# Kernel optimization log

Hardware: AMD Instinct MI355X
Metric: run time of the kernel (lower is better)

Reference implementation:

```python
import jax, jax.numpy as jnp
import numpy as np

NUM_PEAK = 28000
NUM_GENE = 12000
N_NODES = NUM_PEAK + NUM_GENE
N_EDGES = 640000
NUM_TOPICS = 100
T_HIDDEN = 512
EMB = 64
HID = 128  # 2 * emb_size, hidden_channels of GCN
BATCH = 256
BN_EPS = 1e-5


def setup_inputs() -> dict:
    key = jax.random.key(0)
    ks = iter(jax.random.split(key, 64))
    def nrm(shape, s=0.05):
        return jax.random.normal(next(ks), shape, dtype=jnp.float32) * s
    def unif(shape):
        return jax.random.uniform(next(ks), shape, dtype=jnp.float32)
    z = lambda *s: jnp.zeros(s, jnp.float32)
    o = lambda *s: jnp.ones(s, jnp.float32)
    inp = dict(
        Gene=unif((BATCH, NUM_GENE)),
        Gene_normalized=unif((BATCH, NUM_GENE)),
        Peak=unif((BATCH, NUM_PEAK)),
        Peak_normalized=unif((BATCH, NUM_PEAK)),
        feature_matrix=nrm((N_NODES, EMB), 1.0),
        # GATv2 layer 1 (EMB -> HID, heads=1)
        Wl1=nrm((HID, EMB)), bl1=z(HID), Wr1=nrm((HID, EMB)), br1=z(HID),
        att1=nrm((HID,), 0.1), bias1=z(HID),
        # GATv2 layer 2 (HID -> EMB)
        Wl2=nrm((EMB, HID)), bl2=z(EMB), Wr2=nrm((EMB, HID)), br2=z(EMB),
        att2=nrm((EMB,), 0.1), bias2=z(EMB),
        # gene encoder: Linear + ReLU + BN + Linear + ReLU + BN
        gW1=nrm((T_HIDDEN, NUM_GENE)), gb1=z(T_HIDDEN), gg1=o(T_HIDDEN), gbe1=z(T_HIDDEN),
        gW2=nrm((T_HIDDEN, T_HIDDEN)), gb2=z(T_HIDDEN), gg2=o(T_HIDDEN), gbe2=z(T_HIDDEN),
        # peak encoder
        pW1=nrm((T_HIDDEN, NUM_PEAK)), pb1=z(T_HIDDEN), pg1=o(T_HIDDEN), pbe1=z(T_HIDDEN),
        pW2=nrm((T_HIDDEN, T_HIDDEN)), pb2=z(T_HIDDEN), pg2=o(T_HIDDEN), pbe2=z(T_HIDDEN),
        mu_W=nrm((NUM_TOPICS, T_HIDDEN)), mu_b=z(NUM_TOPICS),
        ls_W=nrm((NUM_TOPICS, T_HIDDEN)), ls_b=z(NUM_TOPICS),
        alphas_W=nrm((NUM_TOPICS, EMB)),
        alphas_star_W=nrm((NUM_TOPICS, EMB)),
        edge_index=jax.random.randint(next(ks), (2, N_EDGES), 0, N_NODES),
    )
    return inp


def _batchnorm(h, gamma, beta):
    # training-style BN over batch axis (biased variance), eps=1e-5
    m = h.mean(axis=0)
    v = jnp.mean((h - m) ** 2, axis=0)
    return (h - m) * jax.lax.rsqrt(v + BN_EPS) * gamma + beta


def _gatv2(x, src, dst, Wl, bl, Wr, br, att, bias):
    # PyG GATv2Conv, heads=1: e_ij = att . leaky_relu(Wl x_j + Wr x_i),
    # softmax over incoming edges of i, out_i = sum_j alpha_ij * (Wl x_j) + bias
    xl = x @ Wl.T + bl            # [N, C]
    xr = x @ Wr.T + br            # [N, C]
    e = jax.nn.leaky_relu(xl[src] + xr[dst], negative_slope=0.2)  # [E, C]
    logit = e @ att               # [E]
    m = jax.ops.segment_max(logit, dst, num_segments=N_NODES)
    ex = jnp.exp(logit - m[dst])
    den = jax.ops.segment_sum(ex, dst, num_segments=N_NODES)
    alpha = ex / (den[dst] + 1e-16)
    out = jax.ops.segment_sum(alpha[:, None] * xl[src], dst, num_segments=N_NODES)
    return out + bias


def _encode(x, W1, b1, g1, be1, W2, b2, g2, be2, mu_W, mu_b, ls_W, ls_b):
    h = _batchnorm(jax.nn.relu(x @ W1.T + b1), g1, be1)
    h = _batchnorm(jax.nn.relu(h @ W2.T + b2), g2, be2)
    mu = h @ mu_W.T + mu_b
    logsigma = 2.0 * (h @ ls_W.T + ls_b)
    kl = -0.5 * jnp.sum(1.0 + logsigma - mu ** 2 - jnp.exp(logsigma), axis=-1).mean()
    return mu, kl


def reference(Gene, Gene_normalized, Peak, Peak_normalized, feature_matrix,
              Wl1, bl1, Wr1, br1, att1, bias1,
              Wl2, bl2, Wr2, br2, att2, bias2,
              gW1, gb1, gg1, gbe1, gW2, gb2, gg2, gbe2,
              pW1, pb1, pg1, pbe1, pW2, pb2, pg2, pbe2,
              mu_W, mu_b, ls_W, ls_b, alphas_W, alphas_star_W, edge_index):
    # ---- variational encoders (eval mode: dropout off, theta from mu) ----
    mu_d, kl_d = _encode(Gene_normalized, gW1, gb1, gg1, gbe1, gW2, gb2, gg2, gbe2,
                         mu_W, mu_b, ls_W, ls_b)
    mu_j, kl_j = _encode(Peak_normalized, pW1, pb1, pg1, pbe1, pW2, pb2, pg2, pbe2,
                         mu_W, mu_b, ls_W, ls_b)
    theta_d = jax.nn.softmax(mu_d, axis=-1)   # [B, K]
    theta_j = jax.nn.softmax(mu_j, axis=-1)
    kld_theta = kl_d + kl_j

    # ---- GCN embedding: two GATv2Conv layers with self-loops ----
    loops = jnp.arange(N_NODES)
    src = jnp.concatenate([edge_index[0], loops])
    dst = jnp.concatenate([edge_index[1], loops])
    h = jax.nn.relu(_gatv2(feature_matrix, src, dst, Wl1, bl1, Wr1, br1, att1, bias1))
    emb = _gatv2(h, src, dst, Wl2, bl2, Wr2, br2, att2, bias2)
    emb = jax.nn.relu(emb)  # theta_act applied in forward
    eta_matrix = emb[:NUM_PEAK]   # [num_peak, EMB]
    rho_matrix = emb[NUM_PEAK:]   # [num_gene, EMB]

    # ---- topic-word matrices: softmax over genes/peaks (dim=0), transposed ----
    beta_gene = jax.nn.softmax(rho_matrix @ alphas_W.T, axis=0).T        # [K, num_gene]
    beta_peak = jax.nn.softmax(eta_matrix @ alphas_star_W.T, axis=0).T   # [K, num_peak]

    # ---- decode + reconstruction loss ----
    preds_gene = jnp.log(theta_d @ beta_gene + 1e-6)
    preds_peak = jnp.log(theta_j @ beta_peak + 1e-6)
    recon = (-(preds_gene * Gene).sum(-1) - (preds_peak * Peak).sum(-1)).mean()
    return recon, kld_theta
```

## Files before the change

### kernel.cpp

```cpp
#include <hip/hip_runtime.h>
#include <cstdint>
#include <cstddef>

using u16 = unsigned short;
using u32 = unsigned int;
typedef __attribute__((ext_vector_type(8))) short bf16x8;
typedef __attribute__((ext_vector_type(4))) float f32x4;

static constexpr int NUM_PEAK = 28000;
static constexpr int NUM_GENE = 12000;
static constexpr int N_NODES  = NUM_PEAK + NUM_GENE;
static constexpr int N_EDGES  = 640000;
static constexpr int E_TOTAL  = N_EDGES + N_NODES;
static constexpr int NT       = 100;
static constexpr int NT2      = 200;
static constexpr int NTP      = 128;
static constexpr int TH       = 512;
static constexpr int EMB      = 64;
static constexpr int HID      = 128;
static constexpr int BATCH    = 256;
static constexpr int SCAN_CHUNK = 1024;
static constexpr int SCAN_NB  = (N_NODES + SCAN_CHUNK - 1) / SCAN_CHUNK;
static constexpr int ENC_CH   = 1280;
static constexpr int KPG      = 12032;
static constexpr int KPP      = 28032;
static constexpr int KSPG     = (NUM_GENE + ENC_CH - 1) / ENC_CH;
static constexpr int KSPP     = (NUM_PEAK + ENC_CH - 1) / ENC_CH;
static constexpr int ENC1B    = 8 * 4 * (KSPG + KSPP);
static constexpr int DEGB     = (E_TOTAL + 255) / 256;
static constexpr int PADGB    = BATCH * KPG / 8 / 256;
static constexpr int PADPB    = BATCH * KPP / 8 / 256;
static constexpr int CS_ROWS  = 128;
static constexpr int NBMAX    = (NUM_PEAK + CS_ROWS - 1) / CS_ROWS;
#define BN_EPS 1e-5f

__device__ __forceinline__ u16 f2bf(float f) {
  u32 b = __float_as_uint(f);
  return (u16)((b + 0x7FFFu + ((b >> 16) & 1u)) >> 16);
}

struct CvtJobs {
  const float* src[12];
  u16* dst[12];
  u32 n[12];
  u32 start[12];
  int count;
};

__device__ void dev_cvt_all(const CvtJobs& J, int bid) {
  int seg = 0;
  while (seg + 1 < J.count && bid >= (int)J.start[seg + 1]) ++seg;
  const float* __restrict__ src = J.src[seg];
  u16* __restrict__ dst = J.dst[seg];
  const u32 n = J.n[seg];
  const u32 i = (u32)(bid - J.start[seg]) * 2048u + threadIdx.x * 8u;
  if (i + 8 <= n) {
    float4 a = *(const float4*)(src + i);
    float4 b = *(const float4*)(src + i + 4);
    ushort4 o0{f2bf(a.x), f2bf(a.y), f2bf(a.z), f2bf(a.w)};
    ushort4 o1{f2bf(b.x), f2bf(b.y), f2bf(b.z), f2bf(b.w)};
    *(ushort4*)(dst + i) = o0;
    *(ushort4*)(dst + i + 4) = o1;
  } else {
    for (u32 j = i; j < n; ++j) dst[j] = f2bf(src[j]);
  }
}

__device__ void dev_cvt_pad(const float* __restrict__ src, u16* __restrict__ dst,
                            int K, int Kp, int bid) {
  const size_t i = ((size_t)bid * 256 + threadIdx.x) * 8;
  const int col = (int)(i % Kp);
  const size_t row = i / Kp;
  ushort4 o0{0, 0, 0, 0}, o1{0, 0, 0, 0};
  if (col + 8 <= K) {
    const float* s = src + row * K + col;
    float4 a = *(const float4*)s;
    float4 b = *(const float4*)(s + 4);
    o0 = ushort4{f2bf(a.x), f2bf(a.y), f2bf(a.z), f2bf(a.w)};
    o1 = ushort4{f2bf(b.x), f2bf(b.y), f2bf(b.z), f2bf(b.w)};
  }
  *(ushort4*)(dst + i) = o0;
  *(ushort4*)(dst + i + 4) = o1;
}

__device__ void dev_deg_count(const int* __restrict__ ei, int* __restrict__ deg,
                              int* __restrict__ pos, int bid) {
  const int e = bid * 256 + threadIdx.x;
  if (e >= E_TOTAL) return;
  const int d = (e < N_EDGES) ? ei[N_EDGES + e] : e - N_EDGES;
  pos[e] = atomicAdd(&deg[d], 1);
}

__device__ void dev_csr_scatter(const int* __restrict__ ei,
                                const int* __restrict__ row_ptr,
                                const int* __restrict__ pos,
                                int* __restrict__ csr_src, int bid) {
  const int e = bid * 256 + threadIdx.x;
  if (e >= E_TOTAL) return;
  int s, d;
  if (e < N_EDGES) { s = ei[e]; d = ei[N_EDGES + e]; }
  else { s = d = e - N_EDGES; }
  csr_src[row_ptr[d] + pos[e]] = s;
}

__global__ __launch_bounds__(256) void megaA(
    const int* ei, int* deg, int* pos,
    const float* GeneN, u16* GeneNb, const float* PeakN, u16* PeakNb,
    CvtJobs J) {
  const int bid = blockIdx.x;
  if (bid < DEGB) dev_deg_count(ei, deg, pos, bid);
  else if (bid < DEGB + PADGB) dev_cvt_pad(GeneN, GeneNb, NUM_GENE, KPG, bid - DEGB);
  else if (bid < DEGB + PADGB + PADPB) dev_cvt_pad(PeakN, PeakNb, NUM_PEAK, KPP, bid - DEGB - PADGB);
  else dev_cvt_all(J, bid - DEGB - PADGB - PADPB);
}

struct GP {
  const u16* A; const u16* B; float* C; u16* Cb; const float* bias;
  int M, N, K;
};

__device__ void dev_gemm_bt(const GP g, int bxx, int byy, char* smem) {
  u16 (*As)[40] = (u16(*)[40])smem;
  u16 (*Bs)[40] = (u16(*)[40])(smem + 64 * 40 * 2);
  const int M = g.M, N = g.N, K = g.K;
  const int tid = threadIdx.x;
  const int bm = byy * 64, bn = bxx * 64;
  if (bm >= M || bn >= N) return;
  const int w = tid >> 6, lane = tid & 63;
  const int wm = (w >> 1) * 32, wn = (w & 1) * 32;
  const int fr = lane & 15;
  const int ks = (lane >> 4) * 8;
  const int srow = tid >> 2, sseg = (tid & 3) * 8;
  f32x4 acc[2][2] = {};
  for (int kt = 0; kt < K; kt += 32) {
    const int gk = kt + sseg;
    {
      const int gm = bm + srow;
      bf16x8 v = {0, 0, 0, 0, 0, 0, 0, 0};
      if (gm < M) v = *(const bf16x8*)(g.A + (size_t)gm * K + gk);
      *(bf16x8*)&As[srow][sseg] = v;
    }
    {
      const int gn = bn + srow;
      bf16x8 v = {0, 0, 0, 0, 0, 0, 0, 0};
      if (gn < N) v = *(const bf16x8*)(g.B + (size_t)gn * K + gk);
      *(bf16x8*)&Bs[srow][sseg] = v;
    }
    __syncthreads();
    bf16x8 a0 = *(const bf16x8*)&As[wm + fr][ks];
    bf16x8 a1 = *(const bf16x8*)&As[wm + 16 + fr][ks];
    bf16x8 b0 = *(const bf16x8*)&Bs[wn + fr][ks];
    bf16x8 b1 = *(const bf16x8*)&Bs[wn + 16 + fr][ks];
    acc[0][0] = __builtin_amdgcn_mfma_f32_16x16x32_bf16(a0, b0, acc[0][0], 0, 0, 0);
    acc[0][1] = __builtin_amdgcn_mfma_f32_16x16x32_bf16(a0, b1, acc[0][1], 0, 0, 0);
    acc[1][0] = __builtin_amdgcn_mfma_f32_16x16x32_bf16(a1, b0, acc[1][0], 0, 0, 0);
    acc[1][1] = __builtin_amdgcn_mfma_f32_16x16x32_bf16(a1, b1, acc[1][1], 0, 0, 0);
    __syncthreads();
  }
#pragma unroll
  for (int fi = 0; fi < 2; ++fi)
#pragma unroll
    for (int fj = 0; fj < 2; ++fj)
#pragma unroll
      for (int r = 0; r < 4; ++r) {
        const int row = bm + wm + fi * 16 + (lane >> 4) * 4 + r;
        const int col = bn + wn + fj * 16 + fr;
        if (row < M && col < N) {
          const float v = acc[fi][fj][r];
          if (g.Cb) g.Cb[(size_t)row * N + col] = f2bf(v + (g.bias ? g.bias[col] : 0.f));
          else g.C[(size_t)row * N + col] = v + (g.bias ? g.bias[col] : 0.f);
        }
      }
}

__device__ __forceinline__ int swz64(int row, int colu16) {
  return row * 64 + ((((colu16 >> 3) ^ row) & 7) << 3) + (colu16 & 7);
}

__device__ void dev_enc1(
    const u16* __restrict__ A0, const float* __restrict__ B0, float* __restrict__ P0,
    const u16* __restrict__ A1, const float* __restrict__ B1, float* __restrict__ P1,
    int bid, char* smem) {
  const int cpx = ENC1B >> 3;
  const int f2 = (bid & 7) * cpx + (bid >> 3);
  const int bx = f2 % 8;
  const int by = (f2 / 8) % 4;
  const int bz = f2 / 32;
  const bool second = (bz >= KSPG);
  const u16* __restrict__ A = second ? A1 : A0;
  const float* __restrict__ B = second ? B1 : B0;
  float* __restrict__ P = second ? P1 : P0;
  const int K = second ? NUM_PEAK : NUM_GENE;
  const int Kp = second ? KPP : KPG;
  const int zz = second ? bz - KSPG : bz;
  const int k0 = zz * ENC_CH;
  const int k1 = min(K, k0 + ENC_CH);
  u16* As = (u16*)smem;
  u16* Bs = (u16*)(smem + 8192);
  const int tid = threadIdx.x;
  const int bm = by * 64;
  const int bn = bx * 64;
  const int w = tid >> 6, lane = tid & 63;
  const int wm = w * 16;
  const int fr = lane & 15, g = lane >> 4;
  const int ar = tid >> 2, acol = (tid & 3) * 16;
  const int br = tid >> 2, bcol = (tid & 3) * 16;
  const u16* Abase = A + (size_t)(bm + ar) * Kp + acol;
  const float* Bbase = B + (size_t)(bn + br) * K + bcol;

  bf16x8 rA0, rA1;
  float4 rB0, rB1, rB2, rB3;
  auto LD = [&](int kt) {
    const u16* sa = Abase + kt;
    rA0 = *(const bf16x8*)(sa);
    rA1 = *(const bf16x8*)(sa + 8);
    if (kt + bcol + 16 <= K) {
      const float* sb = Bbase + kt;
      rB0 = *(const float4*)(sb);
      rB1 = *(const float4*)(sb + 4);
      rB2 = *(const float4*)(sb + 8);
      rB3 = *(const float4*)(sb + 12);
    } else {
      rB0 = float4{0.f, 0.f, 0.f, 0.f}; rB1 = rB0; rB2 = rB0; rB3 = rB0;
    }
  };
  auto ST = [&]() {
    *(bf16x8*)&As[swz64(ar, acol)] = rA0;
    *(bf16x8*)&As[swz64(ar, acol + 8)] = rA1;
    ushort4 p0{f2bf(rB0.x), f2bf(rB0.y), f2bf(rB0.z), f2bf(rB0.w)};
    ushort4 p1{f2bf(rB1.x), f2bf(rB1.y), f2bf(rB1.z), f2bf(rB1.w)};
    ushort4 p2{f2bf(rB2.x), f2bf(rB2.y), f2bf(rB2.z), f2bf(rB2.w)};
    ushort4 p3{f2bf(rB3.x), f2bf(rB3.y), f2bf(rB3.z), f2bf(rB3.w)};
    const int b0 = swz64(br, bcol);
    const int b1 = swz64(br, bcol + 8);
    *(ushort4*)&Bs[b0] = p0;
    *(ushort4*)&Bs[b0 + 4] = p1;
    *(ushort4*)&Bs[b1] = p2;
    *(ushort4*)&Bs[b1 + 4] = p3;
  };

  f32x4 acc[4] = {};
  LD(k0);
  ST();
  for (int kt = k0; kt < k1; kt += 64) {
    __syncthreads();
    const bool more = (kt + 64 < k1);
    if (more) LD(kt + 64);
#pragma unroll
    for (int s = 0; s < 2; ++s) {
      const int kc = s * 32 + g * 8;
      bf16x8 a = *(const bf16x8*)&As[swz64(wm + fr, kc)];
#pragma unroll
      for (int fj = 0; fj < 4; ++fj) {
        bf16x8 b = *(const bf16x8*)&Bs[swz64(fj * 16 + fr, kc)];
        acc[fj] = __builtin_amdgcn_mfma_f32_16x16x32_bf16(a, b, acc[fj], 0, 0, 0);
      }
    }
    __syncthreads();
    if (more) ST();
  }
  float* Pz = P + (size_t)zz * TH * 256;
  const int row = bm + wm + g * 4;
#pragma unroll
  for (int fj = 0; fj < 4; ++fj) {
    const int col = bn + fj * 16 + fr;
    *(f32x4*)&Pz[(size_t)col * 256 + row] = acc[fj];
  }
}

template <int C>
__device__ void dev_gat(
    const u16* __restrict__ xl, const u16* __restrict__ xr,
    const float* __restrict__ att, const float* __restrict__ bias,
    const int* __restrict__ row_ptr, const int* __restrict__ csr_src,
    u16* __restrict__ out_b, int blk) {
  constexpr int CPL = C / 8;
  constexpr int W = CPL / 2;
  const int lane = threadIdx.x & 63;
  const int g = lane >> 3, li = lane & 7;
  const int d = blk * 4 + ((int)threadIdx.x >> 6);
  if (d >= N_NODES) return;
  const int c0 = li * CPL;
  float xrv[CPL], attv[CPL], acc[CPL];
  {
    const u32* xrw = (const u32*)(xr + (size_t)d * C + c0);
#pragma unroll
    for (int i = 0; i < W; ++i) {
      const u32 wv = xrw[i];
      xrv[2 * i]     = __uint_as_float(wv << 16);
      xrv[2 * i + 1] = __uint_as_float(wv & 0xffff0000u);
    }
  }
#pragma unroll
  for (int i = 0; i < CPL; ++i) { attv[i] = att[c0 + i]; acc[i] = 0.f; }
  float m = -INFINITY, den = 0.f;
  const int end = row_ptr[d + 1];
  int p = row_ptr[d] + g;
  int s = (p < end) ? csr_src[p] : 0;
  u32 w[W];
  {
    const u32* sw = (const u32*)(xl + (size_t)s * C + c0);
#pragma unroll
    for (int i = 0; i < W; ++i) w[i] = sw[i];
  }
  while (p < end) {
    const int sn = (p + 8 < end) ? csr_src[p + 8] : 0;
    u32 wn[W];
    {
      const u32* sw = (const u32*)(xl + (size_t)sn * C + c0);
#pragma unroll
      for (int i = 0; i < W; ++i) wn[i] = sw[i];
    }
    float xlv[CPL];
#pragma unroll
    for (int i = 0; i < W; ++i) {
      xlv[2 * i]     = __uint_as_float(w[i] << 16);
      xlv[2 * i + 1] = __uint_as_float(w[i] & 0xffff0000u);
    }
    float part = 0.f;
#pragma unroll
    for (int i = 0; i < CPL; ++i) {
      float x = xlv[i] + xrv[i];
      x = (x > 0.f) ? x : 0.2f * x;
      part += x * attv[i];
    }
    part += __shfl_xor(part, 1);
    part += __shfl_xor(part, 2);
    part += __shfl_xor(part, 4);
    const float nm = fmaxf(m, part);
    const float scale = __expf(m - nm);
    const float ex = __expf(part - nm);
    den = den * scale + ex;
#pragma unroll
    for (int i = 0; i < CPL; ++i) acc[i] = acc[i] * scale + ex * xlv[i];
    m = nm;
    p += 8;
#pragma unroll
    for (int i = 0; i < W; ++i) w[i] = wn[i];
  }
  float M = m;
  M = fmaxf(M, __shfl_xor(M, 8));
  M = fmaxf(M, __shfl_xor(M, 16));
  M = fmaxf(M, __shfl_xor(M, 32));
  const float gs = __expf(m - M);
  den *= gs;
  den += __shfl_xor(den, 8);
  den += __shfl_xor(den, 16);
  den += __shfl_xor(den, 32);
  const float inv = 1.f / (den + 1e-16f);
  float va[CPL];
#pragma unroll
  for (int i = 0; i < CPL; ++i) {
    float a = acc[i] * gs;
    a += __shfl_xor(a, 8);
    a += __shfl_xor(a, 16);
    a += __shfl_xor(a, 32);
    va[i] = a;
  }
  if (g == 0) {
    u32* dst = (u32*)(out_b + (size_t)d * C + c0);
#pragma unroll
    for (int i = 0; i < W; ++i) {
      const u16 lo = f2bf(fmaxf(va[2 * i] * inv + bias[c0 + 2 * i], 0.f));
      const u16 hi = f2bf(fmaxf(va[2 * i + 1] * inv + bias[c0 + 2 * i + 1], 0.f));
      dst[i] = (u32)lo | ((u32)hi << 16);
    }
  }
}

__device__ void dev_bn_body(float v, const float* gma, const float* be, int c,
                            u16* ob, float* red) {
  const int r = threadIdx.x;
  red[r] = v; __syncthreads();
  for (int s = BATCH / 2; s > 0; s >>= 1) { if (r < s) red[r] += red[r + s]; __syncthreads(); }
  const float mean = red[0] * (1.f / BATCH);
  __syncthreads();
  const float d = v - mean;
  red[r] = d * d; __syncthreads();
  for (int s = BATCH / 2; s > 0; s >>= 1) { if (r < s) red[r] += red[r + s]; __syncthreads(); }
  const float var = red[0] * (1.f / BATCH);
  ob[(size_t)r * TH + c] = f2bf(d * rsqrtf(var + BN_EPS) * gma[c] + be[c]);
}

__device__ void dev_bn_part(
    int cg, const float* __restrict__ PG, int nzG, const float* bg,
    const float* gg, const float* beg, u16* og,
    const float* __restrict__ PP, int nzP, const float* bp,
    const float* gp, const float* bep, u16* op, float* red) {
  int c = cg;
  const float *P, *b, *gma, *be; u16* ob; int nz;
  if (c < TH) { P = PG; nz = nzG; b = bg; gma = gg; be = beg; ob = og; }
  else { c -= TH; P = PP; nz = nzP; b = bp; gma = gp; be = bep; ob = op; }
  const int r = threadIdx.x;
  float v = 0.f;
  const float* base = P + (size_t)c * 256 + r;
  for (int z = 0; z < nz; ++z) v += base[(size_t)z * TH * 256];
  v = fmaxf(v + b[c], 0.f);
  dev_bn_body(v, gma, be, c, ob, red);
}

__device__ void dev_bn2(
    int cg, const float* __restrict__ Hg, const float* bg,
    const float* gg, const float* beg, u16* og,
    const float* __restrict__ Hp, const float* bp,
    const float* gp, const float* bep, u16* op, float* red) {
  int c = cg;
  const float *H, *b, *gma, *be; u16* ob;
  if (c < TH) { H = Hg; b = bg; gma = gg; be = beg; ob = og; }
  else { c -= TH; H = Hp; b = bp; gma = gp; be = bep; ob = op; }
  const int r = threadIdx.x;
  float v = fmaxf(H[(size_t)r * TH + c] + b[c], 0.f);
  dev_bn_body(v, gma, be, c, ob, red);
}

__device__ void dev_row_kl(
    int b, int which, const float* __restrict__ mld, const float* __restrict__ mlj,
    const float* mu_b, const float* ls_b,
    u16* thd, u16* thj, float* kl_out, float* red) {
  const float* ml = which ? mlj : mld;
  u16* thb = which ? thj : thd;
  const int t = threadIdx.x;
  const bool act = (t < NT);
  float mu = 0.f, ls = 0.f, term = 0.f;
  if (act) {
    mu = ml[(size_t)b * NT2 + t] + mu_b[t];
    ls = 2.f * (ml[(size_t)b * NT2 + NT + t] + ls_b[t]);
    term = 1.f + ls - mu * mu - expf(ls);
  }
  red[t] = act ? term : 0.f; __syncthreads();
  for (int s = 64; s > 0; s >>= 1) { if (t < s) red[t] += red[t + s]; __syncthreads(); }
  if (t == 0) atomicAdd(kl_out, -0.5f * red[0] * (1.f / BATCH));
  __syncthreads();
  red[t] = act ? mu : -INFINITY; __syncthreads();
  for (int s = 64; s > 0; s >>= 1) { if (t < s) red[t] = fmaxf(red[t], red[t + s]); __syncthreads(); }
  const float mx = red[0];
  __syncthreads();
  const float e = act ? expf(mu - mx) : 0.f;
  red[t] = e; __syncthreads();
  for (int s = 64; s > 0; s >>= 1) { if (t < s) red[t] += red[t + s]; __syncthreads(); }
  thb[(size_t)b * NTP + t] = act ? f2bf(e / red[0]) : (u16)0;
}

__device__ void dev_col_stats(
    int bx, int sec, const float* __restrict__ Lg, const float* __restrict__ Lp,
    float* __restrict__ bstats) {
  const float* L = sec ? Lp : Lg;
  const int M = sec ? NUM_PEAK : NUM_GENE;
  const int r0 = bx * CS_ROWS;
  const int c = threadIdx.x;
  if (c >= NT || r0 >= M) return;
  const int rend = min(r0 + CS_ROWS, M);
  float m = -INFINITY, s = 0.f;
  for (int r = r0; r < rend; ++r) {
    const float v = L[(size_t)r * NT + c];
    const float nm = fmaxf(m, v);
    s = s * __expf(m - nm) + __expf(v - nm);
    m = nm;
  }
  float* bs = bstats + (((size_t)sec * NT + c) * NBMAX + bx) * 2;
  bs[0] = m;
  bs[1] = s;
}

__global__ __launch_bounds__(256) void mega1(
    const u16* A0, const float* B0, float* P0,
    const u16* A1, const float* B1, float* P1,
    GP l, GP r,
    const int* ei, const int* row_ptr, const int* pos, int* csr_src) {
  __shared__ __align__(16) char smem[20480];
  const int bid = blockIdx.x;
  if (bid < ENC1B) {
    dev_enc1(A0, B0, P0, A1, B1, P1, bid, smem);
  } else if (bid < ENC1B + 2500) {
    const int sub = bid - ENC1B;
    const GP& g = (sub >= 1250) ? r : l;
    const int rem = sub % 1250;
    dev_gemm_bt(g, rem % 2, rem / 2, smem);
  } else {
    dev_csr_scatter(ei, row_ptr, pos, csr_src, bid - ENC1B - 2500);
  }
}

__global__ __launch_bounds__(256) void mega2(
    const float* PG, int nzG, const float* bg, const float* gg, const float* beg, u16* og,
    const float* PP, int nzP, const float* bp, const float* gp, const float* bep, u16* op,
    const u16* xl, const u16* xr, const float* att, const float* bias,
    const int* row_ptr, const int* csr_src, u16* out_b) {
  __shared__ float red[256];
  const int bid = blockIdx.x;
  if (bid < 2 * TH)
    dev_bn_part(bid, PG, nzG, bg, gg, beg, og, PP, nzP, bp, gp, bep, op, red);
  else
    dev_gat<HID>(xl, xr, att, bias, row_ptr, csr_src, out_b, bid - 2 * TH);
}

__global__ __launch_bounds__(256) void mega3(GP eg, GP ep, GP l, GP r) {
  __shared__ __align__(16) char smem[20480];
  const int bid = blockIdx.x;
  if (bid < 64) {
    const int z = bid >> 5, rem = bid & 31;
    dev_gemm_bt(z ? ep : eg, rem & 7, rem >> 3, smem);
  } else {
    const int sub = bid - 64;
    const GP& g = (sub >= 625) ? r : l;
    dev_gemm_bt(g, 0, sub % 625, smem);
  }
}

__global__ __launch_bounds__(256) void mega4(
    const float* Hg, const float* bg, const float* gg, const float* beg, u16* og,
    const float* Hp, const float* bp, const float* gp, const float* bep, u16* op,
    const u16* xl, const u16* xr, const float* att, const float* bias,
    const int* row_ptr, const int* csr_src, u16* out_b) {
  __shared__ float red[256];
  const int bid = blockIdx.x;
  if (bid < 2 * TH)
    dev_bn2(bid, Hg, bg, gg, beg, og, Hp, bp, gp, bep, op, red);
  else
    dev_gat<EMB>(xl, xr, att, bias, row_ptr, csr_src, out_b, bid - 2 * TH);
}

__global__ __launch_bounds__(256) void mega5(GP hg, GP hp, GP tg, GP tp) {
  __shared__ __align__(16) char smem[20480];
  const int bid = blockIdx.x;
  if (bid < 32) {
    const int z = bid >> 4, rem = bid & 15;
    dev_gemm_bt(z ? hp : hg, rem & 3, rem >> 2, smem);
  } else {
    const int sub = bid - 32;
    const GP& g = (sub >= 876) ? tp : tg;
    const int rem = sub % 876;
    dev_gemm_bt(g, rem & 1, rem >> 1, smem);
  }
}

__global__ __launch_bounds__(128) void mega6(
    const float* mld, const float* mlj, const float* mu_b, const float* ls_b,
    u16* thd, u16* thj, float* kl_out,
    const float* Lg, const float* Lp, float* bstats) {
  __shared__ float red[128];
  const int bid = blockIdx.x;
  if (bid < 2 * BATCH)
    dev_row_kl(bid % BATCH, bid / BATCH, mld, mlj, mu_b, ls_b, thd, thj, kl_out, red);
  else {
    const int sub = bid - 2 * BATCH;
    dev_col_stats(sub % NBMAX, sub / NBMAX, Lg, Lp, bstats);
  }
}

__global__ __launch_bounds__(256) void scan_part(
    const int* __restrict__ deg, int* __restrict__ bsum) {
  const int base = blockIdx.x * SCAN_CHUNK + threadIdx.x * 4;
  int s = 0;
#pragma unroll
  for (int i = 0; i < 4; ++i) {
    const int idx = base + i;
    if (idx < N_NODES) s += deg[idx];
  }
  for (int o = 32; o > 0; o >>= 1) s += __shfl_down(s, o);
  __shared__ int ws[4];
  if ((threadIdx.x & 63) == 0) ws[threadIdx.x >> 6] = s;
  __syncthreads();
  if (threadIdx.x == 0) bsum[blockIdx.x] = ws[0] + ws[1] + ws[2] + ws[3];
}

__global__ __launch_bounds__(64) void scan_bsum(int* __restrict__ bsum) {
  if (threadIdx.x == 0) {
    int run = 0;
    for (int i = 0; i < SCAN_NB; ++i) { int v = bsum[i]; bsum[i] = run; run += v; }
  }
}

__global__ __launch_bounds__(256) void scan_final(
    const int* __restrict__ deg, const int* __restrict__ bsum,
    int* __restrict__ row_ptr) {
  const int t = threadIdx.x;
  const int base = blockIdx.x * SCAN_CHUNK + t * 4;
  int v[4], s = 0;
#pragma unroll
  for (int i = 0; i < 4; ++i) {
    const int idx = base + i;
    v[i] = (idx < N_NODES) ? deg[idx] : 0;
    s += v[i];
  }
  const int lane = t & 63, w = t >> 6;
  int x = s;
  for (int o = 1; o < 64; o <<= 1) {
    int y = __shfl_up(x, o);
    if (lane >= o) x += y;
  }
  __shared__ int wtot[4];
  if (lane == 63) wtot[w] = x;
  __syncthreads();
  int woff = 0;
  for (int i = 0; i < w; ++i) woff += wtot[i];
  int excl = bsum[blockIdx.x] + woff + x - s;
#pragma unroll
  for (int i = 0; i < 4; ++i) {
    const int idx = base + i;
    if (idx < N_NODES) { row_ptr[idx] = excl; excl += v[i]; }
  }
  if (blockIdx.x == 0 && t == 0) row_ptr[N_NODES] = E_TOTAL;
}

__global__ __launch_bounds__(64) void col_merge(
    const float* __restrict__ bstats, int nbG, int nbP,
    float* __restrict__ mstat, float* __restrict__ istat) {
  const bool sec = (blockIdx.y != 0);
  const int nb = sec ? nbP : nbG;
  const int c = blockIdx.x;
  const int l = threadIdx.x;
  const float* bs = bstats + ((size_t)blockIdx.y * NT + c) * NBMAX * 2;
  float m = -INFINITY, s = 0.f;
  for (int b = l; b < nb; b += 64) {
    const float mb = bs[b * 2];
    const float sb = bs[b * 2 + 1];
    const float nm = fmaxf(m, mb);
    s = s * __expf(m - nm) + sb * __expf(mb - nm);
    m = nm;
  }
#pragma unroll
  for (int o = 32; o > 0; o >>= 1) {
    const float mo = __shfl_xor(m, o);
    const float so = __shfl_xor(s, o);
    const float nm = fmaxf(m, mo);
    s = s * __expf(m - nm) + so * __expf(mo - nm);
    m = nm;
  }
  if (l == 0) {
    mstat[blockIdx.y * NT + c] = m;
    istat[blockIdx.y * NT + c] = 1.f / s;
  }
}

__global__ __launch_bounds__(256) void beta_norm(
    const float* __restrict__ Lg, const float* __restrict__ Lp,
    const float* __restrict__ mstat, const float* __restrict__ istat,
    u16* __restrict__ og, u16* __restrict__ op) {
  const float* L = blockIdx.y ? Lp : Lg;
  const int M = blockIdx.y ? NUM_PEAK : NUM_GENE;
  const float* mxg = mstat + blockIdx.y * NT;
  const float* ivg = istat + blockIdx.y * NT;
  u16* o = blockIdx.y ? op : og;
  __shared__ float mx[NT], inv[NT];
  for (int i = threadIdx.x; i < NT; i += 256) { mx[i] = mxg[i]; inv[i] = ivg[i]; }
  __syncthreads();
  const size_t total = (size_t)M * NTP;
  size_t i = (size_t)blockIdx.x * 256 + threadIdx.x;
  const size_t stride = (size_t)gridDim.x * 256;
  for (; i < total; i += stride) {
    const int c = (int)(i & (NTP - 1));
    u16 v = 0;
    if (c < NT) {
      const size_t r = i >> 7;
      v = f2bf(__expf(L[r * NT + c] - mx[c]) * inv[c]);
    }
    o[i] = v;
  }
}

__global__ __launch_bounds__(256) void recon_fused(
    const u16* __restrict__ thg, const u16* __restrict__ betag,
    const float* __restrict__ Xg, int Ng, int tiles_g,
    const u16* __restrict__ thp, const u16* __restrict__ betap,
    const float* __restrict__ Xp, int Np, float* __restrict__ partials) {
  __shared__ float pred[64][65];
  __shared__ float wsum[4];
  int ct = blockIdx.x;
  const u16* A; const u16* B; const float* X; int N;
  if (ct < tiles_g) { A = thg; B = betag; X = Xg; N = Ng; }
  else { ct -= tiles_g; A = thp; B = betap; X = Xp; N = Np; }
  const int bm = blockIdx.y * 64, bn = ct * 64;
  const int tid = threadIdx.x, w = tid >> 6, lane = tid & 63;
  const int wm = (w >> 1) * 32, wn = (w & 1) * 32;
  const int fr = lane & 15, ks = (lane >> 4) * 8;
  const u16* Ar0 = A + (size_t)(bm + wm + fr) * NTP;
  const u16* Ar1 = A + (size_t)(bm + wm + 16 + fr) * NTP;
  bf16x8 a0[4], a1[4];
#pragma unroll
  for (int kt = 0; kt < 4; ++kt) {
    a0[kt] = *(const bf16x8*)(Ar0 + kt * 32 + ks);
    a1[kt] = *(const bf16x8*)(Ar1 + kt * 32 + ks);
  }
  const int gn0 = min(bn + wn + fr, N - 1);
  const int gn1 = min(bn + wn + 16 + fr, N - 1);
  const u16* Br0 = B + (size_t)gn0 * NTP;
  const u16* Br1 = B + (size_t)gn1 * NTP;
  f32x4 acc[2][2] = {};
#pragma unroll
  for (int kt = 0; kt < 4; ++kt) {
    bf16x8 b0 = *(const bf16x8*)(Br0 + kt * 32 + ks);
    bf16x8 b1 = *(const bf16x8*)(Br1 + kt * 32 + ks);
    acc[0][0] = __builtin_amdgcn_mfma_f32_16x16x32_bf16(a0[kt], b0, acc[0][0], 0, 0, 0);
    acc[0][1] = __builtin_amdgcn_mfma_f32_16x16x32_bf16(a0[kt], b1, acc[0][1], 0, 0, 0);
    acc[1][0] = __builtin_amdgcn_mfma_f32_16x16x32_bf16(a1[kt], b0, acc[1][0], 0, 0, 0);
    acc[1][1] = __builtin_amdgcn_mfma_f32_16x16x32_bf16(a1[kt], b1, acc[1][1], 0, 0, 0);
  }
#pragma unroll
  for (int fi = 0; fi < 2; ++fi)
#pragma unroll
    for (int fj = 0; fj < 2; ++fj)
#pragma unroll
      for (int r = 0; r < 4; ++r)
        pred[wm + fi * 16 + (lane >> 4) * 4 + r][wn + fj * 16 + fr] = acc[fi][fj][r];
  __syncthreads();
  float local = 0.f;
  if (bn + 64 <= N) {
#pragma unroll
    for (int k = 0; k < 4; ++k) {
      const int j = k * 1024 + tid * 4;
      const int row = j >> 6, col = j & 63;
      const float4 xv = *(const float4*)(X + (size_t)(bm + row) * N + bn + col);
      local += xv.x * __logf(pred[row][col + 0] + 1e-6f);
      local += xv.y * __logf(pred[row][col + 1] + 1e-6f);
      local += xv.z * __logf(pred[row][col + 2] + 1e-6f);
      local += xv.w * __logf(pred[row][col + 3] + 1e-6f);
    }
  } else {
#pragma unroll
    for (int k = 0; k < 16; ++k) {
      const int idx = k * 256 + tid, row = idx >> 6, col = idx & 63;
      if (bn + col < N)
        local += X[(size_t)(bm + row) * N + bn + col] * __logf(pred[row][col] + 1e-6f);
    }
  }
  for (int o = 32; o > 0; o >>= 1) local += __shfl_down(local, o);
  if (lane == 0) wsum[w] = local;
  __syncthreads();
  if (tid == 0)
    partials[(size_t)blockIdx.y * gridDim.x + blockIdx.x] =
        wsum[0] + wsum[1] + wsum[2] + wsum[3];
}

__global__ __launch_bounds__(256) void final_recon(
    const float* __restrict__ partials, int n, float* __restrict__ out) {
  float s = 0.f;
  for (int i = threadIdx.x; i < n; i += 256) s += partials[i];
  __shared__ float red[256];
  red[threadIdx.x] = s; __syncthreads();
  for (int o = 128; o > 0; o >>= 1) {
    if (threadIdx.x < o) red[threadIdx.x] += red[threadIdx.x + o];
    __syncthreads();
  }
  if (threadIdx.x == 0) out[0] = -red[0] * (1.f / BATCH);
}

extern "C" void kernel_launch(void* const* d_in, const int* in_sizes, int n_in,
                              void* d_out, int out_size, void* d_ws, size_t ws_size,
                              hipStream_t stream) {
  const float* Gene  = (const float*)d_in[0];
  const float* GeneN = (const float*)d_in[1];
  const float* Peak  = (const float*)d_in[2];
  const float* PeakN = (const float*)d_in[3];
  const float* feat  = (const float*)d_in[4];
  const float* Wl1 = (const float*)d_in[5];  const float* bl1 = (const float*)d_in[6];
  const float* Wr1 = (const float*)d_in[7];  const float* br1 = (const float*)d_in[8];
  const float* att1 = (const float*)d_in[9]; const float* bias1 = (const float*)d_in[10];
  const float* Wl2 = (const float*)d_in[11]; const float* bl2 = (const float*)d_in[12];
  const float* Wr2 = (const float*)d_in[13]; const float* br2 = (const float*)d_in[14];
  const float* att2 = (const float*)d_in[15]; const float* bias2 = (const float*)d_in[16];
  const float* gW1 = (const float*)d_in[17]; const float* gb1 = (const float*)d_in[18];
  const float* gg1 = (const float*)d_in[19]; const float* gbe1 = (const float*)d_in[20];
  const float* gW2 = (const float*)d_in[21]; const float* gb2 = (const float*)d_in[22];
  const float* gg2 = (const float*)d_in[23]; const float* gbe2 = (const float*)d_in[24];
  const float* pW1 = (const float*)d_in[25]; const float* pb1 = (const float*)d_in[26];
  const float* pg1 = (const float*)d_in[27]; const float* pbe1 = (const float*)d_in[28];
  const float* pW2 = (const float*)d_in[29]; const float* pb2 = (const float*)d_in[30];
  const float* pg2 = (const float*)d_in[31]; const float* pbe2 = (const float*)d_in[32];
  const float* mu_W = (const float*)d_in[33]; const float* mu_b = (const float*)d_in[34];
  const float* ls_W = (const float*)d_in[35]; const float* ls_b = (const float*)d_in[36];
  const float* alphas_W = (const float*)d_in[37];
  const float* alphas_star_W = (const float*)d_in[38];
  const int* ei = (const int*)d_in[39];
  float* out = (float*)d_out;
  (void)in_sizes; (void)n_in; (void)ws_size;

  char* base = (char*)d_ws;
  size_t off = 0;
  auto A = [&](size_t bytes) { void* p = base + off; off += (bytes + 255) & ~(size_t)255; return p; };
  int* deg     = (int*)A((size_t)N_NODES * 4);
  int* row_ptr = (int*)A((size_t)(N_NODES + 1) * 4);
  int* bsum    = (int*)A((size_t)(SCAN_NB + 1) * 4);
  int* pos     = (int*)A((size_t)E_TOTAL * 4);
  int* csr_src = (int*)A((size_t)E_TOTAL * 4);
  float* CpartG = (float*)A((size_t)KSPG * TH * 256 * 4);
  float* CpartP = (float*)A((size_t)KSPP * TH * 256 * 4);
  float* h2g = (float*)A((size_t)BATCH * TH * 4);
  float* h2p = (float*)A((size_t)BATCH * TH * 4);
  u16* h1gb = (u16*)A((size_t)BATCH * TH * 2);
  u16* h2gb = (u16*)A((size_t)BATCH * TH * 2);
  u16* h1pb = (u16*)A((size_t)BATCH * TH * 2);
  u16* h2pb = (u16*)A((size_t)BATCH * TH * 2);
  float* ml_d = (float*)A((size_t)BATCH * NT2 * 4);
  float* ml_j = (float*)A((size_t)BATCH * NT2 * 4);
  u16* th_db = (u16*)A((size_t)BATCH * NTP * 2);
  u16* th_jb = (u16*)A((size_t)BATCH * NTP * 2);
  float* lgg = (float*)A((size_t)NUM_GENE * NT * 4);
  float* lgp = (float*)A((size_t)NUM_PEAK * NT * 4);
  u16* betagb = (u16*)A((size_t)NUM_GENE * NTP * 2);
  u16* betapb = (u16*)A((size_t)NUM_PEAK * NTP * 2);
  u16* featb = (u16*)A((size_t)N_NODES * EMB * 2);
  u16* gW2b = (u16*)A((size_t)TH * TH * 2);
  u16* pW2b = (u16*)A((size_t)TH * TH * 2);
  u16* mlWb = (u16*)A((size_t)NT2 * TH * 2);
  u16* Wl1b = (u16*)A((size_t)HID * EMB * 2);
  u16* Wr1b = (u16*)A((size_t)HID * EMB * 2);
  u16* Wl2b = (u16*)A((size_t)EMB * HID * 2);
  u16* Wr2b = (u16*)A((size_t)EMB * HID * 2);
  u16* aWb  = (u16*)A((size_t)NT * EMB * 2);
  u16* aSWb = (u16*)A((size_t)NT * EMB * 2);
  u16* agg1b = (u16*)A((size_t)N_NODES * HID * 2);
  u16* embb  = (u16*)A((size_t)N_NODES * EMB * 2);
  float* mstat = (float*)A(2 * NT * 4);
  float* istat = (float*)A(2 * NT * 4);
  float* bstats = (float*)A((size_t)2 * NT * NBMAX * 2 * 4);
  float* partials = (float*)A(4096 * 4);
  u16* xl1b = (u16*)A((size_t)N_NODES * HID * 2);
  u16* xr1b = (u16*)A((size_t)N_NODES * HID * 2);
  u16* xl2b = (u16*)A((size_t)N_NODES * EMB * 2);
  u16* xr2b = (u16*)A((size_t)N_NODES * EMB * 2);
  u16* GeneNb = (u16*)A((size_t)BATCH * KPG * 2);
  u16* PeakNb = (u16*)A((size_t)BATCH * KPP * 2);

  auto cdiv = [](int a, int b) { return (a + b - 1) / b; };
  auto Z = [&](void* p, size_t bytes) { hipMemsetAsync(p, 0, bytes, stream); };

  Z(d_out, (size_t)out_size * sizeof(float));
  Z(deg, (size_t)N_NODES * 4);

  int cvtallB;
  {
    CvtJobs J = {};
    int c = 0; u32 blocks = 0;
    auto add = [&](const float* s, u16* d, size_t n) {
      J.src[c] = s; J.dst[c] = d; J.n[c] = (u32)n; J.start[c] = blocks;
      blocks += (u32)((n + 2047) / 2048); ++c;
    };
    add(gW2, gW2b, (size_t)TH * TH);
    add(pW2, pW2b, (size_t)TH * TH);
    add(mu_W, mlWb, (size_t)NT * TH);
    add(ls_W, mlWb + (size_t)NT * TH, (size_t)NT * TH);
    add(feat, featb, (size_t)N_NODES * EMB);
    add(Wl1, Wl1b, (size_t)HID * EMB);
    add(Wr1, Wr1b, (size_t)HID * EMB);
    add(Wl2, Wl2b, (size_t)EMB * HID);
    add(Wr2, Wr2b, (size_t)EMB * HID);
    add(alphas_W, aWb, (size_t)NT * EMB);
    add(alphas_star_W, aSWb, (size_t)NT * EMB);
    J.count = c;
    cvtallB = (int)blocks;
    megaA<<<DEGB + PADGB + PADPB + cvtallB, 256, 0, stream>>>(
        ei, deg, pos, GeneN, GeneNb, PeakN, PeakNb, J);
  }

  scan_part<<<SCAN_NB, 256, 0, stream>>>(deg, bsum);
  scan_bsum<<<1, 64, 0, stream>>>(bsum);
  scan_final<<<SCAN_NB, 256, 0, stream>>>(deg, bsum, row_ptr);

  {
    GP l = {featb, Wl1b, nullptr, xl1b, bl1, N_NODES, HID, EMB};
    GP r = {featb, Wr1b, nullptr, xr1b, br1, N_NODES, HID, EMB};
    mega1<<<ENC1B + 2500 + DEGB, 256, 0, stream>>>(
        GeneNb, gW1, CpartG, PeakNb, pW1, CpartP, l, r,
        ei, row_ptr, pos, csr_src);
  }

  mega2<<<2 * TH + N_NODES / 4, 256, 0, stream>>>(
      CpartG, KSPG, gb1, gg1, gbe1, h1gb,
      CpartP, KSPP, pb1, pg1, pbe1, h1pb,
      xl1b, xr1b, att1, bias1, row_ptr, csr_src, agg1b);

  {
    GP eg = {h1gb, gW2b, h2g, nullptr, nullptr, BATCH, TH, TH};
    GP ep = {h1pb, pW2b, h2p, nullptr, nullptr, BATCH, TH, TH};
    GP l  = {agg1b, Wl2b, nullptr, xl2b, bl2, N_NODES, EMB, HID};
    GP r  = {agg1b, Wr2b, nullptr, xr2b, br2, N_NODES, EMB, HID};
    mega3<<<64 + 1250, 256, 0, stream>>>(eg, ep, l, r);
  }

  mega4<<<2 * TH + N_NODES / 4, 256, 0, stream>>>(
      h2g, gb2, gg2, gbe2, h2gb,
      h2p, pb2, pg2, pbe2, h2pb,
      xl2b, xr2b, att2, bias2, row_ptr, csr_src, embb);

  {
    GP hg = {h2gb, mlWb, ml_d, nullptr, nullptr, BATCH, NT2, TH};
    GP hp = {h2pb, mlWb, ml_j, nullptr, nullptr, BATCH, NT2, TH};
    GP tg = {embb + (size_t)NUM_PEAK * EMB, aWb, lgg, nullptr, nullptr, NUM_GENE, NT, EMB};
    GP tp = {embb, aSWb, lgp, nullptr, nullptr, NUM_PEAK, NT, EMB};
    mega5<<<32 + 2 * 2 * 438, 256, 0, stream>>>(hg, hp, tg, tp);
  }

  mega6<<<2 * BATCH + 2 * NBMAX, 128, 0, stream>>>(
      ml_d, ml_j, mu_b, ls_b, th_db, th_jb, out + 1, lgg, lgp, bstats);

  const int nbG = cdiv(NUM_GENE, CS_ROWS);
  const int nbP = cdiv(NUM_PEAK, CS_ROWS);
  col_merge<<<dim3(NT, 2), 64, 0, stream>>>(bstats, nbG, nbP, mstat, istat);
  beta_norm<<<dim3(1024, 2), 256, 0, stream>>>(lgg, lgp, mstat, istat, betagb, betapb);

  const int tiles_g = cdiv(NUM_GENE, 64);
  const int tiles_p = cdiv(NUM_PEAK, 64);
  const int tiles = tiles_g + tiles_p;
  recon_fused<<<dim3(tiles, 4), 256, 0, stream>>>(
      th_db, betagb, Gene, NUM_GENE, tiles_g,
      th_jb, betapb, Peak, NUM_PEAK, partials);
  final_recon<<<1, 256, 0, stream>>>(partials, tiles * 4, out);
}
```

Baseline: 332.1 us.

## Fuse beta softmax normalization into recon GEMM and pad logits to 128 columns

Removes the separate beta_norm kernel, which read the fp32 logits and wrote a padded bf16 beta matrix. The recon kernel now reads the fp32 logits directly and applies exp(x - max) * inv_sum before converting to bf16 for the MFMA operands. To allow aligned float4 loads, the logit GEMM output gets a 128-column stride through a new ldc field, and col_stats is updated to match. This saves a launch and a full write and read of beta. In exchange, the exp work is repeated across the 4 batch-row blocks, and recon loads twice the bytes per element (fp32 instead of bf16).

```diff
diff --git a/kernel.cpp b/kernel.cpp
--- a/kernel.cpp
+++ b/kernel.cpp
@@ -116,7 +116,7 @@
 
 struct GP {
   const u16* A; const u16* B; float* C; u16* Cb; const float* bias;
-  int M, N, K;
+  int M, N, K, ldc;
 };
 
 __device__ void dev_gemm_bt(const GP g, int bxx, int byy, char* smem) {
@@ -167,8 +167,8 @@
         const int col = bn + wn + fj * 16 + fr;
         if (row < M && col < N) {
           const float v = acc[fi][fj][r];
-          if (g.Cb) g.Cb[(size_t)row * N + col] = f2bf(v + (g.bias ? g.bias[col] : 0.f));
-          else g.C[(size_t)row * N + col] = v + (g.bias ? g.bias[col] : 0.f);
+          if (g.Cb) g.Cb[(size_t)row * g.ldc + col] = f2bf(v + (g.bias ? g.bias[col] : 0.f));
+          else g.C[(size_t)row * g.ldc + col] = v + (g.bias ? g.bias[col] : 0.f);
         }
       }
 }
@@ -452,7 +452,7 @@
   const int rend = min(r0 + CS_ROWS, M);
   float m = -INFINITY, s = 0.f;
   for (int r = r0; r < rend; ++r) {
-    const float v = L[(size_t)r * NT + c];
+    const float v = L[(size_t)r * NTP + c];
     const float nm = fmaxf(m, v);
     s = s * __expf(m - nm) + __expf(v - nm);
     m = nm;
@@ -633,45 +633,28 @@
   }
 }
 
-__global__ __launch_bounds__(256) void beta_norm(
-    const float* __restrict__ Lg, const float* __restrict__ Lp,
+__global__ __launch_bounds__(256) void recon_fused(
+    const u16* __restrict__ thg, const float* __restrict__ Lg,
+    const float* __restrict__ Xg, int Ng, int tiles_g,
+    const u16* __restrict__ thp, const float* __restrict__ Lp,
+    const float* __restrict__ Xp, int Np,
     const float* __restrict__ mstat, const float* __restrict__ istat,
-    u16* __restrict__ og, u16* __restrict__ op) {
-  const float* L = blockIdx.y ? Lp : Lg;
-  const int M = blockIdx.y ? NUM_PEAK : NUM_GENE;
-  const float* mxg = mstat + blockIdx.y * NT;
-  const float* ivg = istat + blockIdx.y * NT;
-  u16* o = blockIdx.y ? op : og;
-  __shared__ float mx[NT], inv[NT];
-  for (int i = threadIdx.x; i < NT; i += 256) { mx[i] = mxg[i]; inv[i] = ivg[i]; }
-  __syncthreads();
-  const size_t total = (size_t)M * NTP;
-  size_t i = (size_t)blockIdx.x * 256 + threadIdx.x;
-  const size_t stride = (size_t)gridDim.x * 256;
-  for (; i < total; i += stride) {
-    const int c = (int)(i & (NTP - 1));
-    u16 v = 0;
-    if (c < NT) {
-      const size_t r = i >> 7;
-      v = f2bf(__expf(L[r * NT + c] - mx[c]) * inv[c]);
-    }
-    o[i] = v;
-  }
-}
-
-__global__ __launch_bounds__(256) void recon_fused(
-    const u16* __restrict__ thg, const u16* __restrict__ betag,
-    const float* __restrict__ Xg, int Ng, int tiles_g,
-    const u16* __restrict__ thp, const u16* __restrict__ betap,
-    const float* __restrict__ Xp, int Np, float* __restrict__ partials) {
+    float* __restrict__ partials) {
   __shared__ float pred[64][65];
   __shared__ float wsum[4];
+  __shared__ float mx[NTP], inv[NTP];
   int ct = blockIdx.x;
-  const u16* A; const u16* B; const float* X; int N;
-  if (ct < tiles_g) { A = thg; B = betag; X = Xg; N = Ng; }
-  else { ct -= tiles_g; A = thp; B = betap; X = Xp; N = Np; }
+  const u16* A; const float* L; const float* X; int N, sec;
+  if (ct < tiles_g) { A = thg; L = Lg; X = Xg; N = Ng; sec = 0; }
+  else { ct -= tiles_g; A = thp; L = Lp; X = Xp; N = Np; sec = 1; }
+  const int tid = threadIdx.x;
+  if (tid < NTP) {
+    mx[tid]  = (tid < NT) ? mstat[sec * NT + tid] : 0.f;
+    inv[tid] = (tid < NT) ? istat[sec * NT + tid] : 0.f;
+  }
+  __syncthreads();
   const int bm = blockIdx.y * 64, bn = ct * 64;
-  const int tid = threadIdx.x, w = tid >> 6, lane = tid & 63;
+  const int w = tid >> 6, lane = tid & 63;
   const int wm = (w >> 1) * 32, wn = (w & 1) * 32;
   const int fr = lane & 15, ks = (lane >> 4) * 8;
   const u16* Ar0 = A + (size_t)(bm + wm + fr) * NTP;
@@ -684,13 +667,26 @@
   }
   const int gn0 = min(bn + wn + fr, N - 1);
   const int gn1 = min(bn + wn + 16 + fr, N - 1);
-  const u16* Br0 = B + (size_t)gn0 * NTP;
-  const u16* Br1 = B + (size_t)gn1 * NTP;
+  const float* Lr0 = L + (size_t)gn0 * NTP;
+  const float* Lr1 = L + (size_t)gn1 * NTP;
+  auto ldb = [&](const float* Lrow, int c0) -> bf16x8 {
+    float4 f0 = *(const float4*)(Lrow + c0);
+    float4 f1 = *(const float4*)(Lrow + c0 + 4);
+    float v[8] = {f0.x, f0.y, f0.z, f0.w, f1.x, f1.y, f1.z, f1.w};
+    bf16x8 r;
+#pragma unroll
+    for (int j = 0; j < 8; ++j) {
+      const int c = c0 + j;
+      const float e = (c < NT) ? __expf(v[j] - mx[c]) * inv[c] : 0.f;
+      ((u16*)&r)[j] = f2bf(e);
+    }
+    return r;
+  };
   f32x4 acc[2][2] = {};
 #pragma unroll
   for (int kt = 0; kt < 4; ++kt) {
-    bf16x8 b0 = *(const bf16x8*)(Br0 + kt * 32 + ks);
-    bf16x8 b1 = *(const bf16x8*)(Br1 + kt * 32 + ks);
+    bf16x8 b0 = ldb(Lr0, kt * 32 + ks);
+    bf16x8 b1 = ldb(Lr1, kt * 32 + ks);
     acc[0][0] = __builtin_amdgcn_mfma_f32_16x16x32_bf16(a0[kt], b0, acc[0][0], 0, 0, 0);
     acc[0][1] = __builtin_amdgcn_mfma_f32_16x16x32_bf16(a0[kt], b1, acc[0][1], 0, 0, 0);
     acc[1][0] = __builtin_amdgcn_mfma_f32_16x16x32_bf16(a1[kt], b0, acc[1][0], 0, 0, 0);
@@ -795,10 +791,8 @@
   float* ml_j = (float*)A((size_t)BATCH * NT2 * 4);
   u16* th_db = (u16*)A((size_t)BATCH * NTP * 2);
   u16* th_jb = (u16*)A((size_t)BATCH * NTP * 2);
-  float* lgg = (float*)A((size_t)NUM_GENE * NT * 4);
-  float* lgp = (float*)A((size_t)NUM_PEAK * NT * 4);
-  u16* betagb = (u16*)A((size_t)NUM_GENE * NTP * 2);
-  u16* betapb = (u16*)A((size_t)NUM_PEAK * NTP * 2);
+  float* lgg = (float*)A((size_t)NUM_GENE * NTP * 4);
+  float* lgp = (float*)A((size_t)NUM_PEAK * NTP * 4);
   u16* featb = (u16*)A((size_t)N_NODES * EMB * 2);
   u16* gW2b = (u16*)A((size_t)TH * TH * 2);
   u16* pW2b = (u16*)A((size_t)TH * TH * 2);
@@ -858,8 +852,8 @@
   scan_final<<<SCAN_NB, 256, 0, stream>>>(deg, bsum, row_ptr);
 
   {
-    GP l = {featb, Wl1b, nullptr, xl1b, bl1, N_NODES, HID, EMB};
-    GP r = {featb, Wr1b, nullptr, xr1b, br1, N_NODES, HID, EMB};
+    GP l = {featb, Wl1b, nullptr, xl1b, bl1, N_NODES, HID, EMB, HID};
+    GP r = {featb, Wr1b, nullptr, xr1b, br1, N_NODES, HID, EMB, HID};
     mega1<<<ENC1B + 2500 + DEGB, 256, 0, stream>>>(
         GeneNb, gW1, CpartG, PeakNb, pW1, CpartP, l, r,
         ei, row_ptr, pos, csr_src);
@@ -871,10 +865,10 @@
       xl1b, xr1b, att1, bias1, row_ptr, csr_src, agg1b);
 
   {
-    GP eg = {h1gb, gW2b, h2g, nullptr, nullptr, BATCH, TH, TH};
-    GP ep = {h1pb, pW2b, h2p, nullptr, nullptr, BATCH, TH, TH};
-    GP l  = {agg1b, Wl2b, nullptr, xl2b, bl2, N_NODES, EMB, HID};
-    GP r  = {agg1b, Wr2b, nullptr, xr2b, br2, N_NODES, EMB, HID};
+    GP eg = {h1gb, gW2b, h2g, nullptr, nullptr, BATCH, TH, TH, TH};
+    GP ep = {h1pb, pW2b, h2p, nullptr, nullptr, BATCH, TH, TH, TH};
+    GP l  = {agg1b, Wl2b, nullptr, xl2b, bl2, N_NODES, EMB, HID, EMB};
+    GP r  = {agg1b, Wr2b, nullptr, xr2b, br2, N_NODES, EMB, HID, EMB};
     mega3<<<64 + 1250, 256, 0, stream>>>(eg, ep, l, r);
   }
 
@@ -884,10 +878,10 @@
       xl2b, xr2b, att2, bias2, row_ptr, csr_src, embb);
 
   {
-    GP hg = {h2gb, mlWb, ml_d, nullptr, nullptr, BATCH, NT2, TH};
-    GP hp = {h2pb, mlWb, ml_j, nullptr, nullptr, BATCH, NT2, TH};
-    GP tg = {embb + (size_t)NUM_PEAK * EMB, aWb, lgg, nullptr, nullptr, NUM_GENE, NT, EMB};
-    GP tp = {embb, aSWb, lgp, nullptr, nullptr, NUM_PEAK, NT, EMB};
+    GP hg = {h2gb, mlWb, ml_d, nullptr, nullptr, BATCH, NT2, TH, NT2};
+    GP hp = {h2pb, mlWb, ml_j, nullptr, nullptr, BATCH, NT2, TH, NT2};
+    GP tg = {embb + (size_t)NUM_PEAK * EMB, aWb, lgg, nullptr, nullptr, NUM_GENE, NT, EMB, NTP};
+    GP tp = {embb, aSWb, lgp, nullptr, nullptr, NUM_PEAK, NT, EMB, NTP};
     mega5<<<32 + 2 * 2 * 438, 256, 0, stream>>>(hg, hp, tg, tp);
   }
 
@@ -897,13 +891,12 @@
   const int nbG = cdiv(NUM_GENE, CS_ROWS);
   const int nbP = cdiv(NUM_PEAK, CS_ROWS);
   col_merge<<<dim3(NT, 2), 64, 0, stream>>>(bstats, nbG, nbP, mstat, istat);
-  beta_norm<<<dim3(1024, 2), 256, 0, stream>>>(lgg, lgp, mstat, istat, betagb, betapb);
 
   const int tiles_g = cdiv(NUM_GENE, 64);
   const int tiles_p = cdiv(NUM_PEAK, 64);
   const int tiles = tiles_g + tiles_p;
   recon_fused<<<dim3(tiles, 4), 256, 0, stream>>>(
-      th_db, betagb, Gene, NUM_GENE, tiles_g,
-      th_jb, betapb, Peak, NUM_PEAK, partials);
+      th_db, lgg, Gene, NUM_GENE, tiles_g,
+      th_jb, lgp, Peak, NUM_PEAK, mstat, istat, partials);
   final_recon<<<1, 256, 0, stream>>>(partials, tiles * 4, out);
 }
```

Result: slower. 342.7 us (+3.2%).
